# Performance work log

Hardware: AMD Instinct MI355X
Metric: run time of the kernel (lower is better)

The kernel has to match this reference:

```python
import jax, jax.numpy as jnp
import numpy as np

CONTEXT = 3  # config['context']
B, H, W = 8, 256, 256
NBR = 2 * CONTEXT  # number of similarity branches


def _conv(x, w, b):
    # x: [N, Cin, H, W], w: [Cout, Cin, kh, kw], SAME padding, stride 1
    y = jax.lax.conv_general_dilated(x, w, (1, 1), 'SAME',
                                     dimension_numbers=('NCHW', 'OIHW', 'NCHW'))
    return y + b[None, :, None, None]


def setup_inputs() -> dict:
    key = jax.random.key(0)
    ks = jax.random.split(key, 5)
    x = jax.random.normal(ks[0], (B, 2 * CONTEXT + 1, H, W), dtype=jnp.float32)
    # kaiming-ish scaled inits
    W1 = jax.random.normal(ks[1], (NBR, 64, 2, 3, 3), dtype=jnp.float32) * (2.0 / (64 * 9)) ** 0.5
    b1 = jnp.zeros((NBR, 64), dtype=jnp.float32)
    W2 = jax.random.normal(ks[2], (NBR, 1, 64, 1, 1), dtype=jnp.float32) * (2.0 / 1) ** 0.5 * 0.1
    b2 = jnp.zeros((NBR, 1), dtype=jnp.float32)
    Wm = jax.random.normal(ks[3], (7, 7, 3, 3), dtype=jnp.float32) * (2.0 / (7 * 9)) ** 0.5
    bm = jnp.zeros((7,), dtype=jnp.float32)
    return {'x': x, 'W1': W1, 'b1': b1, 'W2': W2, 'b2': b2, 'Wm': Wm, 'bm': bm}


def reference(x, W1, b1, W2, b2, Wm, bm):
    # mode == 'context' path just returns x; this implements the main path.
    base = x[:, CONTEXT:CONTEXT + 1]                                  # [B,1,H,W]
    checks = jnp.concatenate([x[:, :CONTEXT], x[:, CONTEXT + 1:]], axis=1)  # [B,6,H,W]
    check_e = checks[:, :, None]                                      # [B,6,1,H,W]
    base_e = jnp.broadcast_to(base[:, None], check_e.shape)           # [B,6,1,H,W]
    # channel order: pre-frames -> (base, check); post-frames -> (check, base)
    ch0 = jnp.concatenate([base_e[:, :CONTEXT], check_e[:, CONTEXT:]], axis=2 - 2 + 2)  # placeholder
    ch0 = jnp.concatenate([base_e[:, :CONTEXT], check_e[:, CONTEXT:]], axis=1)
    ch1 = jnp.concatenate([check_e[:, :CONTEXT], base_e[:, CONTEXT:]], axis=1)
    pairs = jnp.concatenate([ch0, ch1], axis=2)                       # [B,6,2,H,W]
    pairs = jnp.swapaxes(pairs, 0, 1)                                 # [6,B,2,H,W]

    def branch(pair, w1, bb1, w2, bb2):
        h = jax.nn.relu(_conv(pair, w1, bb1))                         # [B,64,H,W]
        return jax.nn.sigmoid(_conv(h, w2, bb2))                      # [B,1,H,W]

    sims = jax.vmap(branch)(pairs, W1, b1, W2, b2)                    # [6,B,1,H,W]
    weighted = sims[:, :, 0] * jnp.swapaxes(checks, 0, 1)             # [6,B,H,W]
    weighted = jnp.swapaxes(weighted, 0, 1)                           # [B,6,H,W]
    combined = jnp.concatenate([weighted[:, :CONTEXT], base, weighted[:, CONTEXT:]], axis=1)  # [B,7,H,W]
    return _conv(combined, Wm, bm)                                    # [B,7,H,W]
```

## Files before the change

kernel.cpp:

```cpp
#include <hip/hip_runtime.h>
#include <math.h>

#define Bn 8
#define Hn 256
#define Wn 256
#define HW (Hn * Wn)
#define ROWS 4
#define RPL 6
#define RP 264
#define ZW (12 * RP)

typedef __attribute__((ext_vector_type(8))) short bf16x8;
typedef __attribute__((ext_vector_type(4))) float f32x4;
typedef __attribute__((ext_vector_type(2))) float f32x2;

__device__ __forceinline__ unsigned int pk_bits(unsigned int lo,
                                                unsigned int hi) {
  return __builtin_amdgcn_perm(hi, lo, 0x07060302u);
}
__device__ __forceinline__ unsigned int pk_bf16(float lo, float hi) {
  return pk_bits(__float_as_uint(lo), __float_as_uint(hi));
}
__device__ __forceinline__ f32x2 fma2(float s, f32x2 a, f32x2 c) {
  f32x2 sv = {s, s};
  return sv * a + c;
}

__device__ __constant__ const int T0c[8] = {0, 1, 2, 9, 10, 11, 3, 4};
__device__ __constant__ const int T1c[8] = {6, 7, 8, 15, 16, 17, 12, 13};
__device__ __constant__ const int T2c[8] = {5, 14, -1, -1, -1, -1, -1, -1};

__global__ __launch_bounds__(256, 4) void sim_kernel(
    const float* __restrict__ x,
    const float* __restrict__ W1,
    const float* __restrict__ b1,
    const float* __restrict__ W2,
    const float* __restrict__ b2,
    float* __restrict__ comb)
{
  __shared__ float rowsF[12 * RP + 64];
  __shared__ uint4 wq[4][64];

  int bi = blockIdx.x;
  int n  = bi >> 9;
  int b  = (bi >> 6) & 7;
  int h0 = (bi & 63) * ROWS;
  int cc = (n < 3) ? n : n + 1;
  int t = threadIdx.x;

  const float* xb     = x + (size_t)b * 7 * HW;
  const float* basep  = xb + 3 * HW;
  const float* checkp = xb + (size_t)cc * HW;

  {
    int f = t >> 6, qq = (t >> 4) & 3, m = t & 15;
    int bsrc = (n < 3) ? 0 : 1;
    const float* wch = W1 + ((size_t)(n * 64 + 16 * f + m)) * 18;
    unsigned int kv[4];
#pragma unroll
    for (int jj = 0; jj < 4; ++jj) {
      int ja = 2 * jj, jb = 2 * jj + 1;
      int ta = (qq == 0) ? T0c[ja] : (qq == 1) ? T1c[ja]
               : (qq == 2) ? T2c[ja] : -1;
      int tb = (qq == 0) ? T0c[jb] : (qq == 1) ? T1c[jb]
               : (qq == 2) ? T2c[jb] : -1;
      float va = 0.f, vb = 0.f;
      if (ta >= 0) {
        int pl = ta / 9, rem = ta - pl * 9;
        va = wch[(pl ? 1 - bsrc : bsrc) * 9 + rem];
      }
      if (tb >= 0) {
        int pl = tb / 9, rem = tb - pl * 9;
        vb = wch[(pl ? 1 - bsrc : bsrc) * 9 + rem];
      }
      kv[jj] = pk_bf16(va, vb);
    }
    wq[f][(qq << 4) + m] = make_uint4(kv[0], kv[1], kv[2], kv[3]);
  }

  int lane = t & 63, wvid = t >> 6;
  int q = lane >> 4, m_ = lane & 15;
  f32x2 w2A[4], w2B[4];
  f32x4 b1vv[4];
#pragma unroll
  for (int f = 0; f < 4; ++f) {
    float4 tw = *(const float4*)&W2[n * 64 + 16 * f + 4 * q];
    float4 tb = *(const float4*)&b1[n * 64 + 16 * f + 4 * q];
    w2A[f][0] = tw.x; w2A[f][1] = tw.y;
    w2B[f][0] = tw.z; w2B[f][1] = tw.w;
    b1vv[f][0] = tb.x; b1vv[f][1] = tb.y;
    b1vv[f][2] = tb.z; b1vv[f][3] = tb.w;
  }
  float bbl = b2[n] * -1.442695041f;

  {
    int col = (t & 63) << 2;
#pragma unroll
    for (int it = 0; it < 3; ++it) {
      int rf = it * 4 + (t >> 6);
      int pl = (rf >= RPL) ? 1 : 0;
      int j  = rf - pl * RPL;
      int hh = h0 - 1 + j;
      const float* src = pl ? checkp : basep;
      float4 val = make_float4(0.f, 0.f, 0.f, 0.f);
      if ((unsigned)hh < (unsigned)Hn)
        val = *(const float4*)(src + hh * Wn + col);
      *(float4*)&rowsF[rf * RP + 4 + col] = val;
    }
    if (t < 12) {
      rowsF[t * RP + 3] = 0.f;
      rowsF[t * RP + 260] = 0.f;
    }
    if (t >= 192) rowsF[ZW + (t - 192)] = 0.f;
  }

  const unsigned int* rowsU = (const unsigned int*)rowsF;
  unsigned int addr[8];
#pragma unroll
  for (int jh = 0; jh < 8; ++jh) {
    int tap = (q == 0) ? T0c[jh] : (q == 1) ? T1c[jh]
              : (q == 2) ? T2c[jh] : -1;
    if (tap >= 0) {
      int pl = tap / 9, rem = tap - pl * 9;
      int rr = rem / 3, dx = rem - rr * 3;
      addr[jh] = (pl * RPL + rr) * RP + 3 + dx + wvid * 64 + m_;
    } else {
      addr[jh] = (unsigned)ZW;
    }
  }
  unsigned int stepA = (q <= 2) ? (unsigned)RP : 0u;
  unsigned int stepB = (q < 2) ? (unsigned)RP : 0u;
  int bpaddr = ((lane ^ 32) << 2);

  __syncthreads();

  bf16x8 afrag[4];
#pragma unroll
  for (int f = 0; f < 4; ++f) afrag[f] = *(const bf16x8*)&wq[f][lane];

  float* combcc = comb + ((size_t)b * 7 + cc) * HW;
  int pxs = wvid * 64 + lane;
  bool bb1 = (lane & 32) != 0;
  bool bb0 = (lane & 16) != 0;

  auto dots2 = [&](unsigned int woff, float& pA, float& pB) {
    union { unsigned int u[4]; bf16x8 v; } p0, p1;
#pragma unroll
    for (int jj = 0; jj < 4; ++jj) {
      p0.u[jj] = pk_bits(rowsU[addr[2 * jj] + woff],
                         rowsU[addr[2 * jj + 1] + woff]);
      p1.u[jj] = pk_bits(rowsU[addr[2 * jj] + woff + 16],
                         rowsU[addr[2 * jj + 1] + woff + 16]);
    }
    f32x4 acc0[4], acc1[4];
#pragma unroll
    for (int f = 0; f < 4; ++f) {
      acc0[f] = __builtin_amdgcn_mfma_f32_16x16x32_bf16(afrag[f], p0.v,
                                                        b1vv[f], 0, 0, 0);
      acc1[f] = __builtin_amdgcn_mfma_f32_16x16x32_bf16(afrag[f], p1.v,
                                                        b1vv[f], 0, 0, 0);
    }
    f32x2 sA0 = {0.f, 0.f}, sB0 = {0.f, 0.f};
    f32x2 sA1 = {0.f, 0.f}, sB1 = {0.f, 0.f};
#pragma unroll
    for (int f = 0; f < 4; ++f) {
      f32x2 a01, a23, c01, c23;
      a01[0] = acc0[f][0]; a01[1] = acc0[f][1];
      a23[0] = acc0[f][2]; a23[1] = acc0[f][3];
      c01[0] = acc1[f][0]; c01[1] = acc1[f][1];
      c23[0] = acc1[f][2]; c23[1] = acc1[f][3];
      a01 = __builtin_elementwise_max(a01, (f32x2)0.f);
      a23 = __builtin_elementwise_max(a23, (f32x2)0.f);
      c01 = __builtin_elementwise_max(c01, (f32x2)0.f);
      c23 = __builtin_elementwise_max(c23, (f32x2)0.f);
      sA0 += w2A[f] * a01;
      sB0 += w2B[f] * a23;
      sA1 += w2A[f] * c01;
      sB1 += w2B[f] * c23;
    }
    f32x2 s0 = sA0 + sB0, s1 = sA1 + sB1;
    pA = s0[0] + s0[1];
    pB = s1[0] + s1[1];
  };

#pragma unroll 1
  for (int r = 0; r < ROWS; ++r) {
    float ccv = rowsF[(RPL + r + 1) * RP + 4 + pxs];

    float P0, P1, P2, P3;
    dots2(0u, P0, P1);
    dots2(32u, P2, P3);

    float U0 = bb1 ? P0 : P2;
    float U1 = bb1 ? P1 : P3;
    float r0 = __int_as_float(
        __builtin_amdgcn_ds_bpermute(bpaddr, __float_as_int(U0)));
    float r1 = __int_as_float(
        __builtin_amdgcn_ds_bpermute(bpaddr, __float_as_int(U1)));
    float T0 = (bb1 ? P2 : P0) + r0;
    float T1 = (bb1 ? P3 : P1) + r1;
    float Wv = bb0 ? T0 : T1;
    float r2 = __int_as_float(
        __builtin_amdgcn_ds_swizzle(__float_as_int(Wv), 0x401F));
    float S = (bb0 ? T1 : T0) + r2;

    float e = __builtin_amdgcn_exp2f(fmaf(S, -1.442695041f, bbl));
    float g = __builtin_amdgcn_rcpf(1.f + e);
    combcc[(h0 + r) * Wn + pxs] = g * ccv;

    if (r < ROWS - 1) {
#pragma unroll
      for (int jh = 0; jh < 8; ++jh) addr[jh] += (jh < 2) ? stepA : stepB;
    }
  }
}

__global__ __launch_bounds__(512) void mix_kernel(
    const float* __restrict__ comb,
    const float* __restrict__ x,
    const float* __restrict__ Wm,
    const float* __restrict__ bm,
    float* __restrict__ out)
{
  __shared__ float mr[42 * RP];

  int bi = blockIdx.x;
  int b  = bi >> 6;
  int h0 = (bi & 63) << 2;
  int t = threadIdx.x;

  for (int u = t; u < 42 * 64; u += 512) {
    int rf = u >> 6;
    int col = (u & 63) << 2;
    int ic = rf / 6, j = rf - ic * 6;
    int hh = h0 - 1 + j;
    const float* src = (ic == 3) ? (x + ((size_t)b * 7 + 3) * HW)
                                 : (comb + ((size_t)b * 7 + ic) * HW);
    float4 v = make_float4(0.f, 0.f, 0.f, 0.f);
    if ((unsigned)hh < (unsigned)Hn)
      v = *(const float4*)(src + hh * Wn + col);
    *(float4*)&mr[rf * RP + 4 + col] = v;
  }
  if (t < 42) {
    mr[t * RP + 3] = 0.f;
    mr[t * RP + 260] = 0.f;
  }
  __syncthreads();

  int r   = t >> 7;
  int px0 = (t & 127) << 1;
  int h   = h0 + r;

  f32x2 acc[7];
#pragma unroll
  for (int oc = 0; oc < 7; ++oc) {
    float bv = bm[oc];
    acc[oc] = (f32x2){bv, bv};
  }

#pragma unroll 1
  for (int ic = 0; ic < 7; ++ic) {
    f32x2 PP[3][3];
#pragma unroll
    for (int dy = 0; dy < 3; ++dy) {
      const float* rp = &mr[(ic * 6 + r + dy) * RP + 3 + px0];
      float v0 = rp[0], v1 = rp[1], v2 = rp[2], v3 = rp[3];
      PP[dy][0] = (f32x2){v0, v1};
      PP[dy][1] = (f32x2){v1, v2};
      PP[dy][2] = (f32x2){v2, v3};
    }
    const float* wp = Wm + ic * 9;
#pragma unroll
    for (int oc = 0; oc < 7; ++oc) {
      const float* wo = wp + oc * 63;
#pragma unroll
      for (int dy = 0; dy < 3; ++dy) {
        float w0 = wo[dy * 3], w1 = wo[dy * 3 + 1], w2 = wo[dy * 3 + 2];
        acc[oc] = fma2(w0, PP[dy][0],
                   fma2(w1, PP[dy][1], fma2(w2, PP[dy][2], acc[oc])));
      }
    }
  }

  float* ob = out + (size_t)b * 7 * HW + h * Wn + px0;
#pragma unroll
  for (int oc = 0; oc < 7; ++oc)
    *(float2*)(ob + (size_t)oc * HW) = make_float2(acc[oc][0], acc[oc][1]);
}

extern "C" void kernel_launch(void* const* d_in, const int* in_sizes, int n_in,
                              void* d_out, int out_size, void* d_ws, size_t ws_size,
                              hipStream_t stream) {
  const float* x  = (const float*)d_in[0];
  const float* W1 = (const float*)d_in[1];
  const float* b1 = (const float*)d_in[2];
  const float* W2 = (const float*)d_in[3];
  const float* b2 = (const float*)d_in[4];
  const float* Wm = (const float*)d_in[5];
  const float* bm = (const float*)d_in[6];
  float* out  = (float*)d_out;
  float* comb = (float*)d_ws;

  sim_kernel<<<6 * 8 * (Hn / ROWS), 256, 0, stream>>>(x, W1, b1, W2, b2, comb);
  mix_kernel<<<8 * (Hn / 4), 512, 0, stream>>>(comb, x, Wm, bm, out);
}
```

Before: 113.2 us.

## Regroup conv taps by column to reuse LDS rows across output rows

The conv taps are reassigned to MFMA K slots so that each lane group holds one (plane, dx) column across three vertical rows, rather than a scattered table of taps. The weight packing and LDS addressing are rebuilt to match, and the per-tap constant tables are removed. A three-row rolling register window now carries loaded LDS values from one output row to the next, so each row loads only one new row of data. This cuts LDS reads per output row. The cost is extra registers for the window and one duplicated slot per group that is multiplied by a zero weight.

```diff
diff --git a/kernel.cpp b/kernel.cpp
--- a/kernel.cpp
+++ b/kernel.cpp
@@ -26,9 +26,6 @@
   return sv * a + c;
 }
 
-__device__ __constant__ const int T0c[8] = {0, 1, 2, 9, 10, 11, 3, 4};
-__device__ __constant__ const int T1c[8] = {6, 7, 8, 15, 16, 17, 12, 13};
-__device__ __constant__ const int T2c[8] = {5, 14, -1, -1, -1, -1, -1, -1};
 
 __global__ __launch_bounds__(256, 4) void sim_kernel(
     const float* __restrict__ x,
@@ -56,25 +53,23 @@
     int f = t >> 6, qq = (t >> 4) & 3, m = t & 15;
     int bsrc = (n < 3) ? 0 : 1;
     const float* wch = W1 + ((size_t)(n * 64 + 16 * f + m)) * 18;
+    int g0pl = (qq == 2) ? 1 : 0;
+    int g0dx = (qq == 0) ? 0 : (qq == 1) ? 2 : 1;
+    int g1pl = (qq == 0) ? 0 : 1;
+    int g1dx = (qq == 0) ? 1 : (qq == 1) ? 0 : 2;
+    float wg0[3], wg1[3];
+#pragma unroll
+    for (int rrs = 0; rrs < 3; ++rrs) {
+      wg0[rrs] = (qq <= 2)
+          ? wch[(g0pl ? 1 - bsrc : bsrc) * 9 + rrs * 3 + g0dx] : 0.f;
+      wg1[rrs] = (qq <= 2)
+          ? wch[(g1pl ? 1 - bsrc : bsrc) * 9 + rrs * 3 + g1dx] : 0.f;
+    }
     unsigned int kv[4];
-#pragma unroll
-    for (int jj = 0; jj < 4; ++jj) {
-      int ja = 2 * jj, jb = 2 * jj + 1;
-      int ta = (qq == 0) ? T0c[ja] : (qq == 1) ? T1c[ja]
-               : (qq == 2) ? T2c[ja] : -1;
-      int tb = (qq == 0) ? T0c[jb] : (qq == 1) ? T1c[jb]
-               : (qq == 2) ? T2c[jb] : -1;
-      float va = 0.f, vb = 0.f;
-      if (ta >= 0) {
-        int pl = ta / 9, rem = ta - pl * 9;
-        va = wch[(pl ? 1 - bsrc : bsrc) * 9 + rem];
-      }
-      if (tb >= 0) {
-        int pl = tb / 9, rem = tb - pl * 9;
-        vb = wch[(pl ? 1 - bsrc : bsrc) * 9 + rem];
-      }
-      kv[jj] = pk_bf16(va, vb);
-    }
+    kv[0] = pk_bf16(wg0[0], wg0[1]);
+    kv[1] = pk_bf16(wg0[2], 0.f);
+    kv[2] = pk_bf16(wg1[0], wg1[1]);
+    kv[3] = pk_bf16(wg1[2], 0.f);
     wq[f][(qq << 4) + m] = make_uint4(kv[0], kv[1], kv[2], kv[3]);
   }
 
@@ -115,21 +110,20 @@
   }
 
   const unsigned int* rowsU = (const unsigned int*)rowsF;
-  unsigned int addr[8];
-#pragma unroll
-  for (int jh = 0; jh < 8; ++jh) {
-    int tap = (q == 0) ? T0c[jh] : (q == 1) ? T1c[jh]
-              : (q == 2) ? T2c[jh] : -1;
-    if (tap >= 0) {
-      int pl = tap / 9, rem = tap - pl * 9;
-      int rr = rem / 3, dx = rem - rr * 3;
-      addr[jh] = (pl * RPL + rr) * RP + 3 + dx + wvid * 64 + m_;
-    } else {
-      addr[jh] = (unsigned)ZW;
-    }
-  }
-  unsigned int stepA = (q <= 2) ? (unsigned)RP : 0u;
-  unsigned int stepB = (q < 2) ? (unsigned)RP : 0u;
+  int g0pl = (q == 2) ? 1 : 0;
+  int g0dx = (q == 0) ? 0 : (q == 1) ? 2 : 1;
+  int g1pl = (q == 0) ? 0 : 1;
+  int g1dx = (q == 0) ? 1 : (q == 1) ? 0 : 2;
+  unsigned int addrG0, addrG1, step;
+  if (q <= 2) {
+    addrG0 = (unsigned)((g0pl * RPL) * RP + 3 + g0dx + wvid * 64 + m_);
+    addrG1 = (unsigned)((g1pl * RPL) * RP + 3 + g1dx + wvid * 64 + m_);
+    step = (unsigned)RP;
+  } else {
+    addrG0 = (unsigned)ZW;
+    addrG1 = (unsigned)ZW;
+    step = 0u;
+  }
   int bpaddr = ((lane ^ 32) << 2);
 
   __syncthreads();
@@ -143,62 +137,90 @@
   bool bb1 = (lane & 32) != 0;
   bool bb0 = (lane & 16) != 0;
 
-  auto dots2 = [&](unsigned int woff, float& pA, float& pB) {
-    union { unsigned int u[4]; bf16x8 v; } p0, p1;
-#pragma unroll
-    for (int jj = 0; jj < 4; ++jj) {
-      p0.u[jj] = pk_bits(rowsU[addr[2 * jj] + woff],
-                         rowsU[addr[2 * jj + 1] + woff]);
-      p1.u[jj] = pk_bits(rowsU[addr[2 * jj] + woff + 16],
-                         rowsU[addr[2 * jj + 1] + woff + 16]);
-    }
-    f32x4 acc0[4], acc1[4];
-#pragma unroll
-    for (int f = 0; f < 4; ++f) {
-      acc0[f] = __builtin_amdgcn_mfma_f32_16x16x32_bf16(afrag[f], p0.v,
-                                                        b1vv[f], 0, 0, 0);
-      acc1[f] = __builtin_amdgcn_mfma_f32_16x16x32_bf16(afrag[f], p1.v,
-                                                        b1vv[f], 0, 0, 0);
-    }
-    f32x2 sA0 = {0.f, 0.f}, sB0 = {0.f, 0.f};
-    f32x2 sA1 = {0.f, 0.f}, sB1 = {0.f, 0.f};
-#pragma unroll
-    for (int f = 0; f < 4; ++f) {
-      f32x2 a01, a23, c01, c23;
-      a01[0] = acc0[f][0]; a01[1] = acc0[f][1];
-      a23[0] = acc0[f][2]; a23[1] = acc0[f][3];
-      c01[0] = acc1[f][0]; c01[1] = acc1[f][1];
-      c23[0] = acc1[f][2]; c23[1] = acc1[f][3];
-      a01 = __builtin_elementwise_max(a01, (f32x2)0.f);
-      a23 = __builtin_elementwise_max(a23, (f32x2)0.f);
-      c01 = __builtin_elementwise_max(c01, (f32x2)0.f);
-      c23 = __builtin_elementwise_max(c23, (f32x2)0.f);
-      sA0 += w2A[f] * a01;
-      sB0 += w2B[f] * a23;
-      sA1 += w2A[f] * c01;
-      sB1 += w2B[f] * c23;
-    }
-    f32x2 s0 = sA0 + sB0, s1 = sA1 + sB1;
-    pA = s0[0] + s0[1];
-    pB = s1[0] + s1[1];
-  };
+  unsigned int va[3][4], vb[3][4];
+#pragma unroll
+  for (int s = 0; s < 4; s += 2) {
+    va[0][s]     = rowsU[addrG0 + s * 16];
+    va[0][s + 1] = rowsU[addrG0 + s * 16 + 16];
+    vb[0][s]     = rowsU[addrG1 + s * 16];
+    vb[0][s + 1] = rowsU[addrG1 + s * 16 + 16];
+  }
+  addrG0 += step; addrG1 += step;
+#pragma unroll
+  for (int s = 0; s < 4; s += 2) {
+    va[1][s]     = rowsU[addrG0 + s * 16];
+    va[1][s + 1] = rowsU[addrG0 + s * 16 + 16];
+    vb[1][s]     = rowsU[addrG1 + s * 16];
+    vb[1][s + 1] = rowsU[addrG1 + s * 16 + 16];
+  }
+  addrG0 += step; addrG1 += step;
 
 #pragma unroll 1
   for (int r = 0; r < ROWS; ++r) {
     float ccv = rowsF[(RPL + r + 1) * RP + 4 + pxs];
 
-    float P0, P1, P2, P3;
-    dots2(0u, P0, P1);
-    dots2(32u, P2, P3);
-
-    float U0 = bb1 ? P0 : P2;
-    float U1 = bb1 ? P1 : P3;
+#pragma unroll
+    for (int s = 0; s < 4; s += 2) {
+      va[2][s]     = rowsU[addrG0 + s * 16];
+      va[2][s + 1] = rowsU[addrG0 + s * 16 + 16];
+      vb[2][s]     = rowsU[addrG1 + s * 16];
+      vb[2][s + 1] = rowsU[addrG1 + s * 16 + 16];
+    }
+    addrG0 += step; addrG1 += step;
+
+    float P[4];
+#pragma unroll
+    for (int sp = 0; sp < 2; ++sp) {
+      int s0 = 2 * sp, s1 = 2 * sp + 1;
+      union { unsigned int u[4]; bf16x8 v; } u0, u1;
+      u0.u[0] = pk_bits(va[0][s0], va[1][s0]);
+      u0.u[1] = pk_bits(va[2][s0], va[2][s0]);
+      u0.u[2] = pk_bits(vb[0][s0], vb[1][s0]);
+      u0.u[3] = pk_bits(vb[2][s0], vb[2][s0]);
+      u1.u[0] = pk_bits(va[0][s1], va[1][s1]);
+      u1.u[1] = pk_bits(va[2][s1], va[2][s1]);
+      u1.u[2] = pk_bits(vb[0][s1], vb[1][s1]);
+      u1.u[3] = pk_bits(vb[2][s1], vb[2][s1]);
+
+      f32x4 acc0[4], acc1[4];
+#pragma unroll
+      for (int f = 0; f < 4; ++f) {
+        acc0[f] = __builtin_amdgcn_mfma_f32_16x16x32_bf16(afrag[f], u0.v,
+                                                          b1vv[f], 0, 0, 0);
+        acc1[f] = __builtin_amdgcn_mfma_f32_16x16x32_bf16(afrag[f], u1.v,
+                                                          b1vv[f], 0, 0, 0);
+      }
+      f32x2 sA0 = {0.f, 0.f}, sB0 = {0.f, 0.f};
+      f32x2 sA1 = {0.f, 0.f}, sB1 = {0.f, 0.f};
+#pragma unroll
+      for (int f = 0; f < 4; ++f) {
+        f32x2 a01, a23, c01, c23;
+        a01[0] = acc0[f][0]; a01[1] = acc0[f][1];
+        a23[0] = acc0[f][2]; a23[1] = acc0[f][3];
+        c01[0] = acc1[f][0]; c01[1] = acc1[f][1];
+        c23[0] = acc1[f][2]; c23[1] = acc1[f][3];
+        a01 = __builtin_elementwise_max(a01, (f32x2)0.f);
+        a23 = __builtin_elementwise_max(a23, (f32x2)0.f);
+        c01 = __builtin_elementwise_max(c01, (f32x2)0.f);
+        c23 = __builtin_elementwise_max(c23, (f32x2)0.f);
+        sA0 += w2A[f] * a01;
+        sB0 += w2B[f] * a23;
+        sA1 += w2A[f] * c01;
+        sB1 += w2B[f] * c23;
+      }
+      f32x2 s0v = sA0 + sB0, s1v = sA1 + sB1;
+      P[s0] = s0v[0] + s0v[1];
+      P[s1] = s1v[0] + s1v[1];
+    }
+
+    float U0 = bb1 ? P[0] : P[2];
+    float U1 = bb1 ? P[1] : P[3];
     float r0 = __int_as_float(
         __builtin_amdgcn_ds_bpermute(bpaddr, __float_as_int(U0)));
     float r1 = __int_as_float(
         __builtin_amdgcn_ds_bpermute(bpaddr, __float_as_int(U1)));
-    float T0 = (bb1 ? P2 : P0) + r0;
-    float T1 = (bb1 ? P3 : P1) + r1;
+    float T0 = (bb1 ? P[2] : P[0]) + r0;
+    float T1 = (bb1 ? P[3] : P[1]) + r1;
     float Wv = bb0 ? T0 : T1;
     float r2 = __int_as_float(
         __builtin_amdgcn_ds_swizzle(__float_as_int(Wv), 0x401F));
@@ -208,9 +230,10 @@
     float g = __builtin_amdgcn_rcpf(1.f + e);
     combcc[(h0 + r) * Wn + pxs] = g * ccv;
 
-    if (r < ROWS - 1) {
-#pragma unroll
-      for (int jh = 0; jh < 8; ++jh) addr[jh] += (jh < 2) ? stepA : stepB;
+#pragma unroll
+    for (int s = 0; s < 4; ++s) {
+      va[0][s] = va[1][s]; va[1][s] = va[2][s];
+      vb[0][s] = vb[1][s]; vb[1][s] = vb[2][s];
     }
   }
 }
```

After: 112.8 us. No clear change (-0.4%).
